# Optimization experiments

Hardware: AMD Instinct MI355X
Metric: run time of the kernel (lower is better)

Reference implementation:

```python
import jax, jax.numpy as jnp
import numpy as np

B, S, D_IN, D_OUT, H = 2, 2048, 1024, 1024, 16
HD = D_OUT // H


def setup_inputs() -> dict:
    key = jax.random.key(0)
    ks = jax.random.split(key, 6)
    x = jax.random.normal(ks[0], (B, S, D_IN), jnp.float32)
    Wq = jax.random.normal(ks[1], (D_IN, D_OUT), jnp.float32) * 0.02
    Wk = jax.random.normal(ks[2], (D_IN, D_OUT), jnp.float32) * 0.02
    Wv = jax.random.normal(ks[3], (D_IN, D_OUT), jnp.float32) * 0.02
    Wo = jax.random.normal(ks[4], (D_OUT, D_OUT), jnp.float32) * 0.02
    bo = jax.random.normal(ks[5], (D_OUT,), jnp.float32) * 0.02
    return {"x": x, "Wq": Wq, "Wk": Wk, "Wv": Wv, "Wo": Wo, "bo": bo}


def reference(x, Wq, Wk, Wv, Wo, bo):
    b, s, _ = x.shape

    def to_heads(t):  # [b, s, d_out] -> [b, h, s, hd]
        return t.reshape(b, s, H, HD).transpose(0, 2, 1, 3)

    Q = to_heads(x @ Wq)
    K = to_heads(x @ Wk)
    V = to_heads(x @ Wv)

    scale = 1.0 / jnp.sqrt(jnp.asarray(HD, x.dtype))
    scores = jnp.einsum("bhqd,bhkd->bhqk", Q, K) * scale
    causal_mask = jnp.triu(jnp.ones((s, s), dtype=bool), k=1)  # True above diag
    scores = jnp.where(causal_mask, jnp.asarray(-1e6, scores.dtype), scores)
    weights = jax.nn.softmax(scores, axis=-1)  # dropout p=0.0 -> identity
    attn = jnp.einsum("bhqk,bhkd->bhqd", weights, V)  # [b, h, s, hd]
    # Faithful to source: reshape [b,h,s,hd] -> [b,s,d_out] WITHOUT head transpose-back
    attn = attn.reshape(b, s, D_OUT)
    return attn @ Wo + bo
```

## Files before the change

### kernel.cpp

```cpp
#include <hip/hip_runtime.h>
#include <stdint.h>


typedef unsigned short u16;
typedef __attribute__((ext_vector_type(8))) short bf16x8;
typedef __attribute__((ext_vector_type(4))) float f32x4;

#define MFMA_BF16(a, b, c) __builtin_amdgcn_mfma_f32_16x16x32_bf16((a), (b), (c), 0, 0, 0)
#define QSCALE 0.18033688011112042f

__device__ __forceinline__ u16 f2bf(float f) {
  union { float f; unsigned int u; } x; x.f = f;
  unsigned int r = x.u + 0x7fffu + ((x.u >> 16) & 1u);
  return (u16)(r >> 16);
}
__device__ __forceinline__ bf16x8 pack8(float4 a, float4 b) {
  bf16x8 r;
  r[0] = (short)f2bf(a.x); r[1] = (short)f2bf(a.y);
  r[2] = (short)f2bf(a.z); r[3] = (short)f2bf(a.w);
  r[4] = (short)f2bf(b.x); r[5] = (short)f2bf(b.y);
  r[6] = (short)f2bf(b.z); r[7] = (short)f2bf(b.w);
  return r;
}
__device__ __forceinline__ void gload_lds16(const u16* g, u16* l) {
  __builtin_amdgcn_global_load_lds((__attribute__((address_space(1))) void*)g,
                                   (__attribute__((address_space(3))) void*)l, 16, 0, 0);
}

template <int CPR>
__device__ __forceinline__ int sw_off(int r, int c) {
  return (r * CPR + (c ^ (r & (CPR - 1)))) * 8;
}

__global__ __launch_bounds__(1024) void prep(
    const float* __restrict__ x, u16* __restrict__ xb,
    const float* __restrict__ Wq, const float* __restrict__ Wk,
    const float* __restrict__ Wv, const float* __restrict__ Wo,
    u16* __restrict__ WoT, u16* __restrict__ WT3) {
  const int bxg = blockIdx.x, by = blockIdx.y;
  if (bxg >= 128) {
    const int blk = (bxg - 128) * 32 + by;
    const int tid = threadIdx.y * 32 + threadIdx.x;
    const size_t i = ((size_t)blk * 1024 + tid) * 8;
    const float4 a = *(const float4*)&x[i];
    const float4 b2 = *(const float4*)&x[i + 4];
    *(bf16x8*)&xb[i] = pack8(a, b2);
    return;
  }
  __shared__ u16 t[32][33];
  const float* W;
  u16* T;
  int j0, wcol;
  if (bxg < 32) {
    j0 = bxg * 32; wcol = j0; W = Wo; T = WoT;
  } else {
    j0 = (bxg - 32) * 32;
    const int g = j0 >> 10;
    W = (g == 0) ? Wq : (g == 1) ? Wk : Wv;
    T = WT3;
    wcol = j0 & 1023;
  }
  const int k0 = by * 32;
  t[threadIdx.y][threadIdx.x] =
      f2bf(W[(size_t)(k0 + threadIdx.y) * 1024 + wcol + threadIdx.x]);
  __syncthreads();
  T[(size_t)(j0 + threadIdx.y) * 1024 + k0 + threadIdx.x] = t[threadIdx.x][threadIdx.y];
}

__global__ __launch_bounds__(256) void x_to_bf16(const float* __restrict__ x,
                                                 u16* __restrict__ xb) {
  const size_t i = ((size_t)blockIdx.x * 256 + threadIdx.x) * 8;
  const float4 a = *(const float4*)&x[i];
  const float4 b = *(const float4*)&x[i + 4];
  *(bf16x8*)&xb[i] = pack8(a, b);
}

__global__ void transpose_cols(const float* __restrict__ W0, const float* __restrict__ W1,
                               const float* __restrict__ W2, u16* __restrict__ T,
                               int h0, int hsx64) {
  __shared__ u16 t[32][33];
  const int j0 = blockIdx.x * 32;
  const int g = j0 / hsx64;
  const float* W = (g == 0) ? W0 : (g == 1) ? W1 : W2;
  const int wc0 = h0 * 64 + (j0 % hsx64);
  const int k0 = blockIdx.y * 32;
  t[threadIdx.y][threadIdx.x] =
      f2bf(W[(size_t)(k0 + threadIdx.y) * 1024 + wc0 + threadIdx.x]);
  __syncthreads();
  T[(size_t)(j0 + threadIdx.y) * 1024 + k0 + threadIdx.x] = t[threadIdx.x][threadIdx.y];
}

template <int MODE, int AF32>
__global__ __launch_bounds__(256, 2) void gemm_bt(
    const void* __restrict__ Av, const u16* __restrict__ BT,
    void* __restrict__ C0v, u16* __restrict__ C1, u16* __restrict__ C2,
    const float* __restrict__ bias, int M, int N, int K, int hs, int h0) {
  __shared__ __align__(16) u16 lsA[2][128 * 32];
  __shared__ __align__(16) u16 lsB[2][128 * 32];
  const int tid = threadIdx.x, lane = tid & 63, wv = tid >> 6;
  const int quad = lane >> 4, l16 = lane & 15;
  const int m0 = blockIdx.y * 128, n0 = blockIdx.x * 128;
  const int wm = (wv >> 1) * 64, wn = (wv & 1) * 64;
  const int hs64 = hs * 64;
  f32x4 acc[4][4] = {};

  if constexpr (!AF32) {
#pragma unroll
    for (int c = 0; c < 2; ++c) {
      const int P = c * 256 + tid, r = P >> 2;
      const int gcol = ((P & 3) ^ (r & 3)) * 8;
      gload_lds16((const u16*)Av + (size_t)(m0 + r) * K + gcol,
                  &lsA[0][(c * 256 + wv * 64) * 8]);
      gload_lds16(BT + (size_t)(n0 + r) * K + gcol,
                  &lsB[0][(c * 256 + wv * 64) * 8]);
    }
    __syncthreads();
    const int nk = K >> 5;
    for (int kt = 0; kt < nk; ++kt) {
      const int buf = kt & 1;
      if (kt + 1 < nk) {
        const int k1 = (kt + 1) << 5;
#pragma unroll
        for (int c = 0; c < 2; ++c) {
          const int P = c * 256 + tid, r = P >> 2;
          const int gcol = ((P & 3) ^ (r & 3)) * 8;
          gload_lds16((const u16*)Av + (size_t)(m0 + r) * K + k1 + gcol,
                      &lsA[buf ^ 1][(c * 256 + wv * 64) * 8]);
          gload_lds16(BT + (size_t)(n0 + r) * K + k1 + gcol,
                      &lsB[buf ^ 1][(c * 256 + wv * 64) * 8]);
        }
      }
      bf16x8 af[4], bfr[4];
#pragma unroll
      for (int i = 0; i < 4; ++i)
        af[i] = *(const bf16x8*)&lsA[buf][sw_off<4>(wm + i * 16 + l16, quad)];
#pragma unroll
      for (int j = 0; j < 4; ++j)
        bfr[j] = *(const bf16x8*)&lsB[buf][sw_off<4>(wn + j * 16 + l16, quad)];
#pragma unroll
      for (int i = 0; i < 4; ++i)
#pragma unroll
        for (int j = 0; j < 4; ++j) acc[i][j] = MFMA_BF16(af[i], bfr[j], acc[i][j]);
      __syncthreads();
    }
  } else {
    for (int k0 = 0; k0 < K; k0 += 32) {
      bf16x8 va[2], vb[2];
#pragma unroll
      for (int c = 0; c < 2; ++c) {
        const int P = c * 256 + tid, r = P >> 2, cc = P & 3;
        const float* Af = (const float*)Av;
        const float4 a0 = *(const float4*)&Af[(size_t)(m0 + r) * K + k0 + cc * 8];
        const float4 a1 = *(const float4*)&Af[(size_t)(m0 + r) * K + k0 + cc * 8 + 4];
        va[c] = pack8(a0, a1);
        vb[c] = *(const bf16x8*)&BT[(size_t)(n0 + r) * K + k0 + cc * 8];
      }
      __syncthreads();
#pragma unroll
      for (int c = 0; c < 2; ++c) {
        const int P = c * 256 + tid, r = P >> 2, cc = P & 3;
        *(bf16x8*)&lsA[0][sw_off<4>(r, cc)] = va[c];
        *(bf16x8*)&lsB[0][sw_off<4>(r, cc)] = vb[c];
      }
      __syncthreads();
      bf16x8 af[4], bfr[4];
#pragma unroll
      for (int i = 0; i < 4; ++i)
        af[i] = *(const bf16x8*)&lsA[0][sw_off<4>(wm + i * 16 + l16, quad)];
#pragma unroll
      for (int j = 0; j < 4; ++j)
        bfr[j] = *(const bf16x8*)&lsB[0][sw_off<4>(wn + j * 16 + l16, quad)];
#pragma unroll
      for (int i = 0; i < 4; ++i)
#pragma unroll
        for (int j = 0; j < 4; ++j) acc[i][j] = MFMA_BF16(af[i], bfr[j], acc[i][j]);
    }
  }

  if constexpr (MODE == 3) {
#pragma unroll
    for (int j = 0; j < 4; ++j) {
      const int n = n0 + wn + j * 16 + l16;
#pragma unroll
      for (int i = 0; i < 4; ++i) {
        const int mb = m0 + wm + i * 16 + quad * 4;
        const int b = mb >> 11, s0 = mb & 2047;
        if (n < hs64) {
#pragma unroll
          for (int r = 0; r < 4; ++r)
            ((u16*)C0v)[((size_t)b * 2048 + s0 + r) * hs64 + n] =
                f2bf(acc[i][j][r] * QSCALE);
        } else if (n < 2 * hs64) {
#pragma unroll
          for (int r = 0; r < 4; ++r)
            C1[((size_t)b * 2048 + s0 + r) * hs64 + (n - hs64)] = f2bf(acc[i][j][r]);
        } else {
          const int nn = n - 2 * hs64;
          uint2 o;
          o.x = (unsigned)f2bf(acc[i][j][0]) | ((unsigned)f2bf(acc[i][j][1]) << 16);
          o.y = (unsigned)f2bf(acc[i][j][2]) | ((unsigned)f2bf(acc[i][j][3]) << 16);
          *(uint2*)&C2[((size_t)(b * hs + (nn >> 6)) * 64 + (nn & 63)) * 2048 + s0] = o;
        }
      }
    }
  } else {
#pragma unroll
    for (int i = 0; i < 4; ++i)
#pragma unroll
      for (int j = 0; j < 4; ++j) {
        const int n = n0 + wn + j * 16 + l16;
        float bv = 0.f;
        if constexpr (MODE == 1) bv = bias[n];
#pragma unroll
        for (int r = 0; r < 4; ++r) {
          const int m = m0 + wm + i * 16 + quad * 4 + r;
          const int b = (m >= hs * 128) ? 1 : 0;
          const int rp = m - b * hs * 128;
          ((float*)C0v)[(size_t)(b * 2048 + h0 * 128 + rp) * 1024 + n] =
              acc[i][j][r] + bv;
        }
      }
  }
}

__global__ __launch_bounds__(256, 2) void attn_fwd(
    const u16* __restrict__ Qsl, const u16* __restrict__ Ksl,
    const u16* __restrict__ VTsl, u16* __restrict__ A2sl, int hs) {
  __shared__ __align__(16) u16 lsK[2][64 * 64];
  __shared__ __align__(16) u16 lsV[2][64 * 64];
  __shared__ __align__(16) u16 lsP[4][16 * 64];
  __shared__ __align__(16) float scrl[64];
  const int tid = threadIdx.x, lane = tid & 63, wv = tid >> 6;
  const int quad = lane >> 4, l16 = lane & 15;
  const int grp = wv >> 1, wq = wv & 1;

  const int cpx = gridDim.x >> 3;
  const int w = (blockIdx.x & 7) * cpx + (blockIdx.x >> 3);
  const int bh = w >> 4, bx = w & 15;

  const int b = (bh >= hs) ? 1 : 0, hh = bh - b * hs;
  const int hs64 = hs * 64;
  const u16* Qb = Qsl + (size_t)b * 2048 * hs64;
  const u16* Kb = Ksl + (size_t)b * 2048 * hs64;
  const u16* Vb = VTsl + (size_t)(b * hs + hh) * 64 * 2048;
  u16* A2b = A2sl + (size_t)(b * hs + hh) * 2048 * 64;
  u16* lsPw = &lsP[wv][0];
  float* scro = (float*)&lsK[0][0];

  bf16x8 ones;
#pragma unroll
  for (int i = 0; i < 8; ++i) ones[i] = (short)0x3F80;

  const int prow = l16 >> 1;
  const int pb0 = (l16 & 1) << 2;

  const int Pa = tid, ra = Pa >> 3, ca = (Pa & 7) ^ (ra & 7);
  const int Pb2 = 256 + tid, rb = Pb2 >> 3, cb = (Pb2 & 7) ^ (rb & 7);
  const size_t kTileStep = (size_t)64 * hs64;
  const u16* const kBa = Kb + (size_t)ra * hs64 + hh * 64 + ca * 8;
  const u16* const kBb = Kb + (size_t)rb * hs64 + hh * 64 + cb * 8;
  const u16* const vBa = Vb + (size_t)ra * 2048 + ca * 8;
  const u16* const vBb = Vb + (size_t)rb * 2048 + cb * 8;
  const int dA = (wv * 64) * 8;
  const int dB = (256 + wv * 64) * 8;

  for (int half = 0; half < 2; ++half) {
    const int qt = (half == 0) ? bx : 31 - bx;
    const int q0 = qt * 64;

    bf16x8 qf[2][2];
#pragma unroll
    for (int j = 0; j < 2; ++j)
#pragma unroll
      for (int ks = 0; ks < 2; ++ks)
        qf[j][ks] = *(const bf16x8*)&Qb[(size_t)(q0 + wq * 32 + j * 16 + l16) * hs64 +
                                        hh * 64 + ks * 32 + quad * 8];

    f32x4 acc_o[2][4] = {};
    f32x4 acc_l[2] = {};

    const u16* pkA = kBa;
    const u16* pkB = kBb;
    const u16* pvA = vBa;
    const u16* pvB = vBb;

    __syncthreads();
    gload_lds16(pkA, &lsK[0][dA]);
    gload_lds16(pkB, &lsK[0][dB]);
    gload_lds16(pvA, &lsV[0][dA]);
    gload_lds16(pvB, &lsV[0][dB]);

    auto body = [&](int buf, bool domask) {
      f32x4 accs[2][2] = {};
#pragma unroll
      for (int ks = 0; ks < 2; ++ks)
#pragma unroll
        for (int nj = 0; nj < 2; ++nj) {
          const bf16x8 kf = *(const bf16x8*)
              &lsK[buf][sw_off<8>(grp * 32 + nj * 16 + l16, ks * 4 + quad)];
          accs[0][nj] = MFMA_BF16(kf, qf[0][ks], accs[0][nj]);
          accs[1][nj] = MFMA_BF16(kf, qf[1][ks], accs[1][nj]);
        }
#pragma unroll
      for (int j = 0; j < 2; ++j) {
        const int grow = wq * 32 + j * 16 + l16;
#pragma unroll
        for (int nj = 0; nj < 2; ++nj) {
#pragma unroll
          for (int r = 0; r < 4; ++r) {
            float p = exp2f(accs[j][nj][r]);
            if (domask) {
              const int keyb = grp * 32 + nj * 16 + quad * 4;
              p = (keyb + r > grow) ? 0.f : p;
            }
            accs[j][nj][r] = p;
          }
          union { float f; unsigned int u; } t0, t1, t2, t3;
          t0.f = accs[j][nj][0]; t1.f = accs[j][nj][1];
          t2.f = accs[j][nj][2]; t3.f = accs[j][nj][3];
          uint2 wpk;
          wpk.x = (t0.u >> 16) | (t1.u & 0xFFFF0000u);
          wpk.y = (t2.u >> 16) | (t3.u & 0xFFFF0000u);
          const int row = j * 8 + prow;
          const int chunk = (pb0 + 2 * nj + (quad >> 1)) ^ prow;
          *(uint2*)&lsPw[row * 64 + chunk * 8 + (quad & 1) * 4] = wpk;
        }
      }
      bf16x8 pf[2];
#pragma unroll
      for (int j = 0; j < 2; ++j) {
        const int row = j * 8 + prow;
        const int chunk = (pb0 + quad) ^ prow;
        pf[j] = *(const bf16x8*)&lsPw[row * 64 + chunk * 8];
        acc_l[j] = MFMA_BF16(ones, pf[j], acc_l[j]);
      }
#pragma unroll
      for (int njo = 0; njo < 4; ++njo) {
        const bf16x8 vf = *(const bf16x8*)
            &lsV[buf][sw_off<8>(njo * 16 + l16, grp * 4 + quad)];
        acc_o[0][njo] = MFMA_BF16(vf, pf[0], acc_o[0][njo]);
        acc_o[1][njo] = MFMA_BF16(vf, pf[1], acc_o[1][njo]);
      }
    };

    for (int kt = 0; kt < qt; ++kt) {
      const int buf = kt & 1, nb = buf ^ 1;
      __syncthreads();
      pkA += kTileStep; pkB += kTileStep; pvA += 64; pvB += 64;
      gload_lds16(pkA, &lsK[nb][dA]);
      gload_lds16(pkB, &lsK[nb][dB]);
      gload_lds16(pvA, &lsV[nb][dA]);
      gload_lds16(pvB, &lsV[nb][dB]);
      body(buf, false);
    }
    {
      __syncthreads();
      body(qt & 1, true);
    }

    __syncthreads();
    if (grp == 1) {
#pragma unroll
      for (int j = 0; j < 2; ++j) {
#pragma unroll
        for (int njo = 0; njo < 4; ++njo) {
          const int ch = (njo * 4 + quad) ^ l16;
          *(f32x4*)&scro[(size_t)(wq * 32 + j * 16 + l16) * 64 + ch * 4] =
              acc_o[j][njo];
        }
        if (quad == 0) scrl[wq * 32 + j * 16 + l16] = acc_l[j][0];
      }
    }
    __syncthreads();
    if (grp == 0) {
#pragma unroll
      for (int j = 0; j < 2; ++j) {
        const int ql = wq * 32 + j * 16 + l16;
        const float inv = 1.0f / (acc_l[j][0] + scrl[ql]);
#pragma unroll
        for (int njo = 0; njo < 4; ++njo) {
          const int ch = (njo * 4 + quad) ^ l16;
          const f32x4 ob = *(const f32x4*)&scro[(size_t)ql * 64 + ch * 4];
          uint2 o;
          o.x = (unsigned)f2bf((acc_o[j][njo][0] + ob[0]) * inv) |
                ((unsigned)f2bf((acc_o[j][njo][1] + ob[1]) * inv) << 16);
          o.y = (unsigned)f2bf((acc_o[j][njo][2] + ob[2]) * inv) |
                ((unsigned)f2bf((acc_o[j][njo][3] + ob[3]) * inv) << 16);
          *(uint2*)&A2b[(size_t)(q0 + ql) * 64 + njo * 16 + quad * 4] = o;
        }
      }
    }
  }
}

extern "C" void kernel_launch(void* const* d_in, const int* in_sizes, int n_in,
                              void* d_out, int out_size, void* d_ws, size_t ws_size,
                              hipStream_t stream) {
  (void)in_sizes; (void)n_in; (void)out_size;
  const float* x  = (const float*)d_in[0];
  const float* Wq = (const float*)d_in[1];
  const float* Wk = (const float*)d_in[2];
  const float* Wv = (const float*)d_in[3];
  const float* Wo = (const float*)d_in[4];
  const float* bo = (const float*)d_in[5];
  float* out = (float*)d_out;
  char* ws = (char*)d_ws;
  const size_t MB = 1024 * 1024;
  const size_t KB = 1024;

  int hs = 2;
  if      (ws_size >= 2 * MB + 16 * 2432 * KB) hs = 16;
  else if (ws_size >= 2 * MB +  8 * 2432 * KB) hs = 8;
  else if (ws_size >= 2 * MB +  4 * 2432 * KB) hs = 4;

  u16* WoT   = (u16*)(ws);
  u16* Ksl   = (u16*)(ws + 2 * MB);
  u16* VTsl  = (u16*)(ws + 2 * MB + (size_t)hs *  512 * KB);
  u16* A2sl  = (u16*)(ws + 2 * MB + (size_t)hs * 1024 * KB);
  u16* WT3sl = (u16*)(ws + 2 * MB + (size_t)hs * 1536 * KB);
  u16* Qsl   = (u16*)(ws + 2 * MB + (size_t)hs * 1920 * KB);

  if (hs == 16) {
    u16* xb = A2sl;
    prep<<<dim3(144, 32), dim3(32, 32), 0, stream>>>(x, xb, Wq, Wk, Wv, Wo, WoT, WT3sl);
    gemm_bt<3, 0><<<dim3(24, 32), 256, 0, stream>>>(
        (const void*)xb, WT3sl, (void*)Qsl, Ksl, VTsl, nullptr, 4096, 3072, 1024, 16, 0);
    attn_fwd<<<dim3(512), 256, 0, stream>>>(Qsl, Ksl, VTsl, A2sl, 16);
    gemm_bt<1, 0><<<dim3(8, 32), 256, 0, stream>>>(
        (const void*)A2sl, WoT, (void*)out, nullptr, nullptr, bo, 4096, 1024, 1024, 16, 0);
  } else {
    transpose_cols<<<dim3(32, 32), dim3(32, 32), 0, stream>>>(Wo, Wo, Wo, WoT, 0, 1024);
    for (int h0 = 0; h0 < 16; h0 += hs) {
      transpose_cols<<<dim3(6 * hs, 32), dim3(32, 32), 0, stream>>>(Wq, Wk, Wv, WT3sl, h0, hs * 64);
      gemm_bt<3, 1><<<dim3((3 * hs) / 2, 32), 256, 0, stream>>>(
          (const void*)x, WT3sl, (void*)Qsl, Ksl, VTsl, nullptr, 4096, 3 * hs * 64, 1024, hs, h0);
      attn_fwd<<<dim3(16 * 2 * hs), 256, 0, stream>>>(Qsl, Ksl, VTsl, A2sl, hs);
      gemm_bt<1, 0><<<dim3(8, 2 * hs), 256, 0, stream>>>(
          (const void*)A2sl, WoT, (void*)out, nullptr, nullptr, bo, 2 * hs * 128, 1024, 1024, hs, h0);
    }
  }
}
```

Baseline: 185.2 us.

## Software-pipeline attention loop with triple-buffered K/V and QK lookahead

Expands the K/V shared-memory ring from two to three buffers and restructures the attention inner loop so the QK^T MFMAs for the next tile are issued before the softmax and PV of the current tile, with global-to-LDS loads staged two tiles ahead. Score accumulators ping-pong between two register sets. The exp2 call is also swapped for the AMDGPU hardware builtin where available. The aim is to hide LDS/global latency and overlap MFMA with exp work, at the cost of more LDS (which may limit occupancy at two blocks per CU) and more registers.

```diff
diff --git a/kernel.cpp b/kernel.cpp
--- a/kernel.cpp
+++ b/kernel.cpp
@@ -8,6 +8,12 @@
 
 #define MFMA_BF16(a, b, c) __builtin_amdgcn_mfma_f32_16x16x32_bf16((a), (b), (c), 0, 0, 0)
 #define QSCALE 0.18033688011112042f
+
+#if __has_builtin(__builtin_amdgcn_exp2f)
+#define EXP2(x) __builtin_amdgcn_exp2f(x)
+#else
+#define EXP2(x) exp2f(x)
+#endif
 
 __device__ __forceinline__ u16 f2bf(float f) {
   union { float f; unsigned int u; } x; x.f = f;
@@ -226,8 +232,8 @@
 __global__ __launch_bounds__(256, 2) void attn_fwd(
     const u16* __restrict__ Qsl, const u16* __restrict__ Ksl,
     const u16* __restrict__ VTsl, u16* __restrict__ A2sl, int hs) {
-  __shared__ __align__(16) u16 lsK[2][64 * 64];
-  __shared__ __align__(16) u16 lsV[2][64 * 64];
+  __shared__ __align__(16) u16 lsK[3][64 * 64];
+  __shared__ __align__(16) u16 lsV[3][64 * 64];
   __shared__ __align__(16) u16 lsP[4][16 * 64];
   __shared__ __align__(16) float scrl[64];
   const int tid = threadIdx.x, lane = tid & 63, wv = tid >> 6;
@@ -283,24 +289,31 @@
     const u16* pkB = kBb;
     const u16* pvA = vBa;
     const u16* pvB = vBb;
-
-    __syncthreads();
-    gload_lds16(pkA, &lsK[0][dA]);
-    gload_lds16(pkB, &lsK[0][dB]);
-    gload_lds16(pvA, &lsV[0][dA]);
-    gload_lds16(pvB, &lsV[0][dB]);
-
-    auto body = [&](int buf, bool domask) {
-      f32x4 accs[2][2] = {};
+    int bc = 0, bn = 1, bf_ = 2;
+
+    auto stage = [&](int bs) {
+      gload_lds16(pkA, &lsK[bs][dA]);
+      gload_lds16(pkB, &lsK[bs][dB]);
+      gload_lds16(pvA, &lsV[bs][dA]);
+      gload_lds16(pvB, &lsV[bs][dB]);
+      pkA += kTileStep; pkB += kTileStep; pvA += 64; pvB += 64;
+    };
+    auto qk = [&](int bK, f32x4 (&S)[2][2]) {
+#pragma unroll
+      for (int j = 0; j < 2; ++j)
+#pragma unroll
+        for (int nj = 0; nj < 2; ++nj) S[j][nj] = f32x4{0.f, 0.f, 0.f, 0.f};
 #pragma unroll
       for (int ks = 0; ks < 2; ++ks)
 #pragma unroll
         for (int nj = 0; nj < 2; ++nj) {
           const bf16x8 kf = *(const bf16x8*)
-              &lsK[buf][sw_off<8>(grp * 32 + nj * 16 + l16, ks * 4 + quad)];
-          accs[0][nj] = MFMA_BF16(kf, qf[0][ks], accs[0][nj]);
-          accs[1][nj] = MFMA_BF16(kf, qf[1][ks], accs[1][nj]);
-        }
+              &lsK[bK][sw_off<8>(grp * 32 + nj * 16 + l16, ks * 4 + quad)];
+          S[0][nj] = MFMA_BF16(kf, qf[0][ks], S[0][nj]);
+          S[1][nj] = MFMA_BF16(kf, qf[1][ks], S[1][nj]);
+        }
+    };
+    auto smpv = [&](f32x4 (&S)[2][2], int bV, bool domask) {
 #pragma unroll
       for (int j = 0; j < 2; ++j) {
         const int grow = wq * 32 + j * 16 + l16;
@@ -308,16 +321,16 @@
         for (int nj = 0; nj < 2; ++nj) {
 #pragma unroll
           for (int r = 0; r < 4; ++r) {
-            float p = exp2f(accs[j][nj][r]);
+            float p = EXP2(S[j][nj][r]);
             if (domask) {
               const int keyb = grp * 32 + nj * 16 + quad * 4;
               p = (keyb + r > grow) ? 0.f : p;
             }
-            accs[j][nj][r] = p;
+            S[j][nj][r] = p;
           }
           union { float f; unsigned int u; } t0, t1, t2, t3;
-          t0.f = accs[j][nj][0]; t1.f = accs[j][nj][1];
-          t2.f = accs[j][nj][2]; t3.f = accs[j][nj][3];
+          t0.f = S[j][nj][0]; t1.f = S[j][nj][1];
+          t2.f = S[j][nj][2]; t3.f = S[j][nj][3];
           uint2 wpk;
           wpk.x = (t0.u >> 16) | (t1.u & 0xFFFF0000u);
           wpk.y = (t2.u >> 16) | (t3.u & 0xFFFF0000u);
@@ -337,26 +350,32 @@
 #pragma unroll
       for (int njo = 0; njo < 4; ++njo) {
         const bf16x8 vf = *(const bf16x8*)
-            &lsV[buf][sw_off<8>(njo * 16 + l16, grp * 4 + quad)];
+            &lsV[bV][sw_off<8>(njo * 16 + l16, grp * 4 + quad)];
         acc_o[0][njo] = MFMA_BF16(vf, pf[0], acc_o[0][njo]);
         acc_o[1][njo] = MFMA_BF16(vf, pf[1], acc_o[1][njo]);
       }
     };
-
-    for (int kt = 0; kt < qt; ++kt) {
-      const int buf = kt & 1, nb = buf ^ 1;
+    auto step = [&](f32x4 (&Sc)[2][2], f32x4 (&Sn)[2][2], int kt) {
       __syncthreads();
-      pkA += kTileStep; pkB += kTileStep; pvA += 64; pvB += 64;
-      gload_lds16(pkA, &lsK[nb][dA]);
-      gload_lds16(pkB, &lsK[nb][dB]);
-      gload_lds16(pvA, &lsV[nb][dA]);
-      gload_lds16(pvB, &lsV[nb][dB]);
-      body(buf, false);
-    }
-    {
-      __syncthreads();
-      body(qt & 1, true);
-    }
+      if (kt + 2 <= qt) stage(bf_);
+      qk(bn, Sn);
+      smpv(Sc, bc, false);
+      const int t = bc; bc = bn; bn = bf_; bf_ = t;
+    };
+
+    __syncthreads();
+    stage(0);
+    __syncthreads();
+    if (qt >= 1) stage(1);
+
+    f32x4 sA[2][2], sB[2][2];
+    qk(0, sA);
+
+    int kt = 0;
+    while (kt + 1 < qt) { step(sA, sB, kt); step(sB, sA, kt + 1); kt += 2; }
+    bool curA = true;
+    if (kt < qt) { step(sA, sB, kt); curA = false; }
+    if (curA) smpv(sA, bc, true); else smpv(sB, bc, true);
 
     __syncthreads();
     if (grp == 1) {
```

Result: faster. 179.5 us (-3.0%).
